# Optimization experiments

Measured on AMD Instinct MI355X. Metric: run time of the kernel, lower is better.

The kernel has to match this reference:

```python
import jax, jax.numpy as jnp
import numpy as np

# Static segment boundaries: lengths [512,512,512] + remainder -> ranges below
SEG_RANGES = [(0, 512), (512, 1024), (1024, 1536), (1536, 2048)]

B, N, D, H = 8, 2048, 1024, 2048
NUM_SEG = len(SEG_RANGES)


def setup_inputs() -> dict:
    key = jax.random.key(0)
    k_x, k1, k2, k3 = jax.random.split(key, 4)
    scale_in = 1.0 / np.sqrt(D)
    scale_h = 1.0 / np.sqrt(H)
    return {
        "x": jax.random.normal(k_x, (B, N, D), dtype=jnp.float32),
        "w1": jax.random.normal(k1, (NUM_SEG, D, H), dtype=jnp.float32) * scale_in,
        "w3": jax.random.normal(k2, (NUM_SEG, D, H), dtype=jnp.float32) * scale_in,
        "w2": jax.random.normal(k3, (NUM_SEG, H, D), dtype=jnp.float32) * scale_h,
    }


def reference(x, w1, w3, w2):
    # Per-segment independent SwiGLU FFN: out_seg = (silu(x W1) * (x W3)) W2
    outs = []
    for i, (s, e) in enumerate(SEG_RANGES):
        seg = jax.lax.dynamic_slice_in_dim(x, s, e - s, axis=-2)  # [B, L_i, D]
        h = jax.nn.silu(jnp.einsum('bld,dh->blh', seg, w1[i])) \
            * jnp.einsum('bld,dh->blh', seg, w3[i])               # [B, L_i, H]
        outs.append(jnp.einsum('blh,hd->bld', h, w2[i]))          # [B, L_i, D]
    # Segments tile [0, N) exactly, so concat == the .at[s:e].set() scatter loop
    return jnp.concatenate(outs, axis=-2)
```

## Files before the change

kernel.cpp:

```cpp
#include <hip/hip_runtime.h>
#include <hip/hip_bf16.h>

typedef __bf16 bf16_t;
typedef __attribute__((ext_vector_type(8))) __bf16 bf16x8;
typedef __attribute__((ext_vector_type(4))) float f32x4;

#define MFMA16(a, b, c) __builtin_amdgcn_mfma_f32_16x16x32_bf16((a), (b), (c), 0, 0, 0)

__device__ __forceinline__ unsigned short f2bf(float f) {
    bf16_t b = (bf16_t)f;
    return __builtin_bit_cast(unsigned short, b);
}

__device__ __forceinline__ void gload16(const void* g, void* l) {
    __builtin_amdgcn_global_load_lds(
        (const __attribute__((address_space(1))) void*)g,
        (__attribute__((address_space(3))) void*)l,
        16, 0, 0);
}

__device__ __forceinline__ void stage_tile(const bf16_t* __restrict__ g, int ld,
                                           bf16_t* lds, int tid) {
#pragma unroll
    for (int p = 0; p < 4; ++p) {
        int row = p * 32 + (tid >> 3);
        int c = (tid & 7) ^ (row & 7);
        gload16(g + (size_t)row * ld + c * 8, lds + p * 2048 + tid * 8);
    }
}

__device__ __forceinline__ bf16x8 read_frag(const bf16_t* lds, int r, int chunk) {
    int s = chunk ^ (r & 7);
    return *(const bf16x8*)(lds + r * 64 + s * 8);
}

__global__ __launch_bounds__(256) void cvtx(const float* __restrict__ src,
                                            bf16_t* __restrict__ dst) {
    size_t i = ((size_t)blockIdx.x * 256 + threadIdx.x) * 8;
    f32x4 v0 = *(const f32x4*)(src + i);
    f32x4 v1 = *(const f32x4*)(src + i + 4);
    bf16x8 o;
    o[0] = (bf16_t)v0[0]; o[1] = (bf16_t)v0[1];
    o[2] = (bf16_t)v0[2]; o[3] = (bf16_t)v0[3];
    o[4] = (bf16_t)v1[0]; o[5] = (bf16_t)v1[1];
    o[6] = (bf16_t)v1[2]; o[7] = (bf16_t)v1[3];
    *(bf16x8*)(dst + i) = o;
}

__global__ __launch_bounds__(256) void transcvt64(const float* __restrict__ src,
                                                  unsigned short* __restrict__ dst,
                                                  int R, int C) {
    __shared__ __align__(16) unsigned short tile[64][66];
    size_t off = (size_t)blockIdx.z * R * C;
    const float* s = src + off;
    unsigned short* d = dst + off;
    int tr = blockIdx.y * 64, tc = blockIdx.x * 64;
    int tid = threadIdx.x;
    int lr = tid >> 4;
    int lc = (tid & 15) * 4;
#pragma unroll
    for (int p = 0; p < 4; ++p) {
        int r = p * 16 + lr;
        f32x4 v = *(const f32x4*)(s + (size_t)(tr + r) * C + tc + lc);
        tile[r][lc + 0] = f2bf(v[0]); tile[r][lc + 1] = f2bf(v[1]);
        tile[r][lc + 2] = f2bf(v[2]); tile[r][lc + 3] = f2bf(v[3]);
    }
    __syncthreads();
#pragma unroll
    for (int p = 0; p < 4; ++p) {
        int oc = p * 16 + lr;
        ushort4 v;
        v.x = tile[lc + 0][oc]; v.y = tile[lc + 1][oc];
        v.z = tile[lc + 2][oc]; v.w = tile[lc + 3][oc];
        *(ushort4*)(d + (size_t)(tc + oc) * R + tr + lc) = v;
    }
}

__global__ __launch_bounds__(256, 3) void gemm13(const bf16_t* __restrict__ Xb,
                                                 const bf16_t* __restrict__ W1t,
                                                 const bf16_t* __restrict__ W3t,
                                                 bf16_t* __restrict__ Hh,
                                                 int row_base) {
    const int K = 1024, N = 2048;
    int row0 = blockIdx.x * 128;
    int col0 = blockIdx.y * 128;
    int seg = ((row_base + row0) & 2047) >> 9;
    const bf16_t* A  = Xb + (size_t)row0 * K;
    const bf16_t* B1 = W1t + (size_t)seg * N * K + (size_t)col0 * K;
    const bf16_t* B3 = W3t + (size_t)seg * N * K + (size_t)col0 * K;

    __shared__ __align__(16) bf16_t smem[3 * 128 * 64];
    bf16_t* sA  = smem;
    bf16_t* sB1 = smem + 8192;
    bf16_t* sB3 = smem + 16384;

    int tid = threadIdx.x;
    int lane = tid & 63, wave = tid >> 6;
    int wm = wave & 1, wn = wave >> 1;
    int quad = lane >> 4, l16 = lane & 15;

    f32x4 accU[4][4], accV[4][4];
    f32x4 z = {0.f, 0.f, 0.f, 0.f};
#pragma unroll
    for (int i = 0; i < 4; ++i)
#pragma unroll
        for (int j = 0; j < 4; ++j) { accU[i][j] = z; accV[i][j] = z; }

    for (int kt = 0; kt < K / 64; ++kt) {
        __syncthreads();
        stage_tile(A + kt * 64, K, sA, tid);
        stage_tile(B1 + kt * 64, K, sB1, tid);
        stage_tile(B3 + kt * 64, K, sB3, tid);
        __syncthreads();
#pragma unroll
        for (int kk = 0; kk < 2; ++kk) {
            int chunk = kk * 4 + quad;
            bf16x8 af[4], b1f[4], b3f[4];
#pragma unroll
            for (int i = 0; i < 4; ++i) af[i] = read_frag(sA, wm * 64 + i * 16 + l16, chunk);
#pragma unroll
            for (int j = 0; j < 4; ++j) b1f[j] = read_frag(sB1, wn * 64 + j * 16 + l16, chunk);
#pragma unroll
            for (int j = 0; j < 4; ++j) b3f[j] = read_frag(sB3, wn * 64 + j * 16 + l16, chunk);
#pragma unroll
            for (int i = 0; i < 4; ++i)
#pragma unroll
                for (int j = 0; j < 4; ++j) {
                    accU[i][j] = MFMA16(af[i], b1f[j], accU[i][j]);
                    accV[i][j] = MFMA16(af[i], b3f[j], accV[i][j]);
                }
        }
    }

    __syncthreads();
    bf16_t* Ct = smem;
#pragma unroll
    for (int i = 0; i < 4; ++i)
#pragma unroll
        for (int j = 0; j < 4; ++j) {
            int r = wm * 64 + i * 16 + quad * 4;
            int c = wn * 64 + j * 16 + l16;
#pragma unroll
            for (int t = 0; t < 4; ++t) {
                float u = accU[i][j][t];
                float v = accV[i][j][t];
                float h = (u / (1.f + __expf(-u))) * v;
                Ct[(r + t) * 136 + c] = (bf16_t)h;
            }
        }
    __syncthreads();
#pragma unroll
    for (int s = 0; s < 8; ++s) {
        int r = s * 16 + wave * 4 + (lane >> 4);
        int cb = (lane & 15) * 8;
        bf16x8 v = *(const bf16x8*)(Ct + r * 136 + cb);
        *(bf16x8*)(Hh + (size_t)(row0 + r) * N + col0 + cb) = v;
    }
}

__global__ __launch_bounds__(256, 3) void gemm2k(const bf16_t* __restrict__ Hh,
                                                 const bf16_t* __restrict__ W2t,
                                                 float* __restrict__ Outc,
                                                 int row_base) {
    const int K = 2048, N = 1024;
    int row0 = blockIdx.x * 128;
    int col0 = blockIdx.y * 128;
    int seg = ((row_base + row0) & 2047) >> 9;
    const bf16_t* A = Hh + (size_t)row0 * K;
    const bf16_t* B = W2t + (size_t)seg * N * K + (size_t)col0 * K;

    __shared__ __align__(16) float smemf[64 * 130];
    bf16_t* sA = (bf16_t*)smemf;
    bf16_t* sB = sA + 8192;

    int tid = threadIdx.x;
    int lane = tid & 63, wave = tid >> 6;
    int wm = wave & 1, wn = wave >> 1;
    int quad = lane >> 4, l16 = lane & 15;

    f32x4 acc[4][4];
    f32x4 z = {0.f, 0.f, 0.f, 0.f};
#pragma unroll
    for (int i = 0; i < 4; ++i)
#pragma unroll
        for (int j = 0; j < 4; ++j) acc[i][j] = z;

    for (int kt = 0; kt < K / 64; ++kt) {
        __syncthreads();
        stage_tile(A + kt * 64, K, sA, tid);
        stage_tile(B + kt * 64, K, sB, tid);
        __syncthreads();
#pragma unroll
        for (int kk = 0; kk < 2; ++kk) {
            int chunk = kk * 4 + quad;
            bf16x8 af[4], bf[4];
#pragma unroll
            for (int i = 0; i < 4; ++i) af[i] = read_frag(sA, wm * 64 + i * 16 + l16, chunk);
#pragma unroll
            for (int j = 0; j < 4; ++j) bf[j] = read_frag(sB, wn * 64 + j * 16 + l16, chunk);
#pragma unroll
            for (int i = 0; i < 4; ++i)
#pragma unroll
                for (int j = 0; j < 4; ++j)
                    acc[i][j] = MFMA16(af[i], bf[j], acc[i][j]);
        }
    }

    for (int pass = 0; pass < 2; ++pass) {
        __syncthreads();
        if (wm == pass) {
#pragma unroll
            for (int i = 0; i < 4; ++i)
#pragma unroll
                for (int j = 0; j < 4; ++j) {
                    int r = i * 16 + quad * 4;
                    int c = wn * 64 + j * 16 + l16;
#pragma unroll
                    for (int t = 0; t < 4; ++t)
                        smemf[(r + t) * 130 + c] = acc[i][j][t];
                }
        }
        __syncthreads();
#pragma unroll
        for (int s = 0; s < 8; ++s) {
            int r = s * 8 + wave * 2 + (lane >> 5);
            int cb = (lane & 31) * 4;
            f32x4 v = *(const f32x4*)(smemf + r * 130 + cb);
            *(f32x4*)(Outc + (size_t)(row0 + pass * 64 + r) * N + col0 + cb) = v;
        }
    }
}

extern "C" void kernel_launch(void* const* d_in, const int* in_sizes, int n_in,
                              void* d_out, int out_size, void* d_ws, size_t ws_size,
                              hipStream_t stream) {
    const float* x  = (const float*)d_in[0];
    const float* w1 = (const float*)d_in[1];
    const float* w3 = (const float*)d_in[2];
    const float* w2 = (const float*)d_in[3];
    float* out = (float*)d_out;

    const size_t WSEG = (size_t)4 * 1024 * 2048;
    bf16_t* w1t = (bf16_t*)d_ws;
    bf16_t* w3t = w1t + WSEG;
    bf16_t* w2t = w3t + WSEG;
    bf16_t* dyn = w2t + WSEG;

    transcvt64<<<dim3(32, 16, 4), 256, 0, stream>>>(w1, (unsigned short*)w1t, 1024, 2048);
    transcvt64<<<dim3(32, 16, 4), 256, 0, stream>>>(w3, (unsigned short*)w3t, 1024, 2048);
    transcvt64<<<dim3(16, 32, 4), 256, 0, stream>>>(w2, (unsigned short*)w2t, 2048, 1024);

    const int TOTAL_ROWS = 16384;
    size_t wbytes = 3 * WSEG * sizeof(bf16_t);
    size_t avail = (ws_size > wbytes) ? ws_size - wbytes : 0;
    int chunk_rows = TOTAL_ROWS;
    while (chunk_rows > 128 && (size_t)chunk_rows * 6144 > avail)
        chunk_rows >>= 1;

    for (int rb = 0; rb < TOTAL_ROWS; rb += chunk_rows) {
        bf16_t* Xb = dyn;
        bf16_t* Hh = dyn + (size_t)chunk_rows * 1024;
        cvtx<<<chunk_rows / 2, 256, 0, stream>>>(x + (size_t)rb * 1024, Xb);
        gemm13<<<dim3(chunk_rows / 128, 16), 256, 0, stream>>>(
            Xb, w1t, w3t, Hh, rb);
        gemm2k<<<dim3(chunk_rows / 128, 8), 256, 0, stream>>>(
            Hh, w2t, out + (size_t)rb * 1024, rb);
    }
}
```

Before: 424.4 us.

## Rewrite both GEMMs with 512-thread tiles and double-buffered phased LDS pipeline

```diff
diff --git a/kernel.cpp b/kernel.cpp
--- a/kernel.cpp
+++ b/kernel.cpp
@@ -17,21 +17,6 @@
         (const __attribute__((address_space(1))) void*)g,
         (__attribute__((address_space(3))) void*)l,
         16, 0, 0);
-}
-
-__device__ __forceinline__ void stage_tile(const bf16_t* __restrict__ g, int ld,
-                                           bf16_t* lds, int tid) {
-#pragma unroll
-    for (int p = 0; p < 4; ++p) {
-        int row = p * 32 + (tid >> 3);
-        int c = (tid & 7) ^ (row & 7);
-        gload16(g + (size_t)row * ld + c * 8, lds + p * 2048 + tid * 8);
-    }
-}
-
-__device__ __forceinline__ bf16x8 read_frag(const bf16_t* lds, int r, int chunk) {
-    int s = chunk ^ (r & 7);
-    return *(const bf16x8*)(lds + r * 64 + s * 8);
 }
 
 __global__ __launch_bounds__(256) void cvtx(const float* __restrict__ src,
@@ -76,28 +61,42 @@
     }
 }
 
-__global__ __launch_bounds__(256, 3) void gemm13(const bf16_t* __restrict__ Xb,
+
+#define PH_FENCE { __builtin_amdgcn_sched_barrier(0); asm volatile("" ::: "memory"); }
+
+__global__ __launch_bounds__(512, 2) void gemm13(const bf16_t* __restrict__ Xb,
                                                  const bf16_t* __restrict__ W1t,
                                                  const bf16_t* __restrict__ W3t,
                                                  bf16_t* __restrict__ Hh,
                                                  int row_base) {
-    const int K = 1024, N = 2048;
-    int row0 = blockIdx.x * 128;
-    int col0 = blockIdx.y * 128;
+    const int K = 1024, N = 2048, KT = 16;
+    int nwg = gridDim.x, id = blockIdx.x;
+    if ((nwg & 7) == 0) id = (id & 7) * (nwg >> 3) + (id >> 3);
+    int nbx = nwg >> 4;
+    int bx = id % nbx, by = id / nbx;
+    int row0 = bx * 256, col0 = by * 128;
     int seg = ((row_base + row0) & 2047) >> 9;
-    const bf16_t* A  = Xb + (size_t)row0 * K;
-    const bf16_t* B1 = W1t + (size_t)seg * N * K + (size_t)col0 * K;
-    const bf16_t* B3 = W3t + (size_t)seg * N * K + (size_t)col0 * K;
-
-    __shared__ __align__(16) bf16_t smem[3 * 128 * 64];
+    const bf16_t* Ag  = Xb + (size_t)row0 * K;
+    const bf16_t* B1g = W1t + ((size_t)seg * N + col0) * K;
+    const bf16_t* B3g = W3t + ((size_t)seg * N + col0) * K;
+
+    __shared__ __align__(16) bf16_t smem[65536];
     bf16_t* sA  = smem;
-    bf16_t* sB1 = smem + 8192;
-    bf16_t* sB3 = smem + 16384;
-
-    int tid = threadIdx.x;
-    int lane = tid & 63, wave = tid >> 6;
-    int wm = wave & 1, wn = wave >> 1;
+    bf16_t* sB1 = smem + 32768;
+    bf16_t* sB3 = smem + 49152;
+
+    int tid = threadIdx.x, lane = tid & 63, w = tid >> 6;
+    int wm = w >> 1, wn = w & 1;
     int quad = lane >> 4, l16 = lane & 15;
+
+    int r0 = 2 * (tid >> 3) + ((tid >> 2) & 1);
+    int c0 = (tid & 3) ^ ((tid >> 3) & 3);
+    int offG  = r0 * K + c0 * 8;
+    int offG2 = offG + 128 * K;
+
+    int sigRd = ((l16 & 1) << 2) | (quad ^ ((l16 >> 1) & 3));
+    int rdA = (wm * 32 + (l16 >> 1)) * 64 + sigRd * 8;
+    int rdB = (wn * 32 + (l16 >> 1)) * 64 + sigRd * 8;
 
     f32x4 accU[4][4], accV[4][4];
     f32x4 z = {0.f, 0.f, 0.f, 0.f};
@@ -106,31 +105,71 @@
 #pragma unroll
         for (int j = 0; j < 4; ++j) { accU[i][j] = z; accV[i][j] = z; }
 
-    for (int kt = 0; kt < K / 64; ++kt) {
-        __syncthreads();
-        stage_tile(A + kt * 64, K, sA, tid);
-        stage_tile(B1 + kt * 64, K, sB1, tid);
-        stage_tile(B3 + kt * 64, K, sB3, tid);
-        __syncthreads();
-#pragma unroll
-        for (int kk = 0; kk < 2; ++kk) {
-            int chunk = kk * 4 + quad;
-            bf16x8 af[4], b1f[4], b3f[4];
-#pragma unroll
-            for (int i = 0; i < 4; ++i) af[i] = read_frag(sA, wm * 64 + i * 16 + l16, chunk);
-#pragma unroll
-            for (int j = 0; j < 4; ++j) b1f[j] = read_frag(sB1, wn * 64 + j * 16 + l16, chunk);
-#pragma unroll
-            for (int j = 0; j < 4; ++j) b3f[j] = read_frag(sB3, wn * 64 + j * 16 + l16, chunk);
-#pragma unroll
-            for (int i = 0; i < 4; ++i)
-#pragma unroll
-                for (int j = 0; j < 4; ++j) {
-                    accU[i][j] = MFMA16(af[i], b1f[j], accU[i][j]);
-                    accV[i][j] = MFMA16(af[i], b3f[j], accV[i][j]);
-                }
-        }
-    }
+    bf16x8 af0[4], af1[4], bfr[4];
+
+#define STGA13(k0, dst) { gload16(Ag + (k0) + offG, (dst) + tid * 8); \
+                          gload16(Ag + (k0) + offG2, (dst) + 4096 + tid * 8); }
+#define STGB13(gb, k0, dst) { gload16((gb) + (k0) + offG, (dst) + tid * 8); }
+
+#define PH13(d, ks, SBASE, AF, RDA, ACC, STAGE, WAITA) {                        \
+    PH_FENCE;                                                                   \
+    if (RDA) {                                                                  \
+        _Pragma("unroll")                                                       \
+        for (int i_ = 0; i_ < 4; ++i_)                                          \
+            AF[i_] = *(const bf16x8*)(sA + (d) * 16384 + (ks) * 8192 + rdA + i_ * 512); \
+    }                                                                           \
+    _Pragma("unroll")                                                           \
+    for (int j_ = 0; j_ < 4; ++j_)                                              \
+        bfr[j_] = *(const bf16x8*)((SBASE) + (d) * 8192 + (ks) * 4096 + rdB + j_ * 512); \
+    STAGE;                                                                      \
+    WAITA;                                                                      \
+    __builtin_amdgcn_s_barrier();                                               \
+    asm volatile("s_waitcnt lgkmcnt(0)" ::: "memory");                          \
+    __builtin_amdgcn_sched_barrier(0);                                          \
+    __builtin_amdgcn_s_setprio(1);                                              \
+    _Pragma("unroll")                                                           \
+    for (int i_ = 0; i_ < 4; ++i_)                                              \
+        _Pragma("unroll")                                                       \
+        for (int j_ = 0; j_ < 4; ++j_)                                          \
+            ACC[i_][j_] = MFMA16(AF[i_], bfr[j_], ACC[i_][j_]);                 \
+    __builtin_amdgcn_s_setprio(0);                                              \
+    __builtin_amdgcn_s_barrier();                                               \
+}
+
+#define TILE13(d, kn) {                                                         \
+    PH13(d, 0, sB1, af0, 1, accU,                                               \
+         { STGA13(kn, sA + (1 - (d)) * 16384);                                  \
+           STGB13(B1g, kn, sB1 + (1 - (d)) * 8192); },                          \
+         asm volatile("s_waitcnt vmcnt(5)" ::: "memory"));                      \
+    PH13(d, 1, sB1, af1, 1, accU,                                               \
+         { STGA13((kn) + 32, sA + (1 - (d)) * 16384 + 8192);                    \
+           STGB13(B1g, (kn) + 32, sB1 + (1 - (d)) * 8192 + 4096); },            \
+         asm volatile("s_waitcnt vmcnt(7)" ::: "memory"));                      \
+    PH13(d, 0, sB3, af0, 0, accV,                                               \
+         { STGB13(B3g, kn, sB3 + (1 - (d)) * 8192); },                          \
+         asm volatile("s_waitcnt vmcnt(7)" ::: "memory"));                      \
+    PH13(d, 1, sB3, af1, 0, accV,                                               \
+         { STGB13(B3g, (kn) + 32, sB3 + (1 - (d)) * 8192 + 4096); },            \
+         asm volatile("s_waitcnt vmcnt(5)" ::: "memory"));                      \
+}
+
+    STGA13(0, sA); STGB13(B1g, 0, sB1);
+    STGA13(32, sA + 8192); STGB13(B1g, 32, sB1 + 4096);
+    STGB13(B3g, 0, sB3); STGB13(B3g, 32, sB3 + 4096);
+    asm volatile("s_waitcnt vmcnt(5)" ::: "memory");
+    __builtin_amdgcn_s_barrier();
+
+    int kt = 0;
+#pragma unroll 1
+    for (; kt + 2 < KT; kt += 2) {
+        TILE13(0, (kt + 1) * 64);
+        TILE13(1, (kt + 2) * 64);
+    }
+    TILE13(0, (kt + 1) * 64);
+    PH13(1, 0, sB1, af0, 1, accU, , asm volatile("s_waitcnt vmcnt(2)" ::: "memory"));
+    PH13(1, 1, sB1, af1, 1, accU, , asm volatile("s_waitcnt vmcnt(1)" ::: "memory"));
+    PH13(1, 0, sB3, af0, 0, accV, , asm volatile("s_waitcnt vmcnt(0)" ::: "memory"));
+    PH13(1, 1, sB3, af1, 0, accV, , );
 
     __syncthreads();
     bf16_t* Ct = smem;
@@ -151,64 +190,120 @@
     __syncthreads();
 #pragma unroll
     for (int s = 0; s < 8; ++s) {
-        int r = s * 16 + wave * 4 + (lane >> 4);
-        int cb = (lane & 15) * 8;
+        int r = s * 32 + (tid >> 4);
+        int cb = (tid & 15) * 8;
         bf16x8 v = *(const bf16x8*)(Ct + r * 136 + cb);
         *(bf16x8*)(Hh + (size_t)(row0 + r) * N + col0 + cb) = v;
     }
-}
-
-__global__ __launch_bounds__(256, 3) void gemm2k(const bf16_t* __restrict__ Hh,
+#undef TILE13
+#undef PH13
+#undef STGA13
+#undef STGB13
+}
+
+__global__ __launch_bounds__(512, 2) void gemm2k(const bf16_t* __restrict__ Hh,
                                                  const bf16_t* __restrict__ W2t,
                                                  float* __restrict__ Outc,
                                                  int row_base) {
-    const int K = 2048, N = 1024;
-    int row0 = blockIdx.x * 128;
-    int col0 = blockIdx.y * 128;
+    const int K = 2048, N = 1024, KT = 32;
+    int nwg = gridDim.x, id = blockIdx.x;
+    if ((nwg & 7) == 0) id = (id & 7) * (nwg >> 3) + (id >> 3);
+    int nbx = nwg >> 2;
+    int bx = id % nbx, by = id / nbx;
+    int row0 = bx * 256, col0 = by * 256;
     int seg = ((row_base + row0) & 2047) >> 9;
-    const bf16_t* A = Hh + (size_t)row0 * K;
-    const bf16_t* B = W2t + (size_t)seg * N * K + (size_t)col0 * K;
-
-    __shared__ __align__(16) float smemf[64 * 130];
-    bf16_t* sA = (bf16_t*)smemf;
-    bf16_t* sB = sA + 8192;
-
-    int tid = threadIdx.x;
-    int lane = tid & 63, wave = tid >> 6;
-    int wm = wave & 1, wn = wave >> 1;
+    const bf16_t* Ag = Hh + (size_t)row0 * K;
+    const bf16_t* Bg = W2t + ((size_t)seg * N + col0) * K;
+
+    __shared__ __align__(16) bf16_t smem[65536];
+    bf16_t* sA = smem;
+    bf16_t* sB = smem + 32768;
+
+    int tid = threadIdx.x, lane = tid & 63, w = tid >> 6;
+    int wm = w >> 2, wn = w & 3;
     int quad = lane >> 4, l16 = lane & 15;
 
-    f32x4 acc[4][4];
+    int r0 = 2 * (tid >> 3) + ((tid >> 2) & 1);
+    int c0 = (tid & 3) ^ ((tid >> 3) & 3);
+    int offG  = r0 * K + c0 * 8;
+    int offG2 = offG + 128 * K;
+
+    int sigRd = ((l16 & 1) << 2) | (quad ^ ((l16 >> 1) & 3));
+    int rdA = (wm * 64 + (l16 >> 1)) * 64 + sigRd * 8;
+    int rdB = (wn * 32 + (l16 >> 1)) * 64 + sigRd * 8;
+
+    f32x4 acc[8][4];
     f32x4 z = {0.f, 0.f, 0.f, 0.f};
 #pragma unroll
-    for (int i = 0; i < 4; ++i)
+    for (int i = 0; i < 8; ++i)
 #pragma unroll
         for (int j = 0; j < 4; ++j) acc[i][j] = z;
 
-    for (int kt = 0; kt < K / 64; ++kt) {
-        __syncthreads();
-        stage_tile(A + kt * 64, K, sA, tid);
-        stage_tile(B + kt * 64, K, sB, tid);
-        __syncthreads();
-#pragma unroll
-        for (int kk = 0; kk < 2; ++kk) {
-            int chunk = kk * 4 + quad;
-            bf16x8 af[4], bf[4];
-#pragma unroll
-            for (int i = 0; i < 4; ++i) af[i] = read_frag(sA, wm * 64 + i * 16 + l16, chunk);
-#pragma unroll
-            for (int j = 0; j < 4; ++j) bf[j] = read_frag(sB, wn * 64 + j * 16 + l16, chunk);
-#pragma unroll
-            for (int i = 0; i < 4; ++i)
-#pragma unroll
-                for (int j = 0; j < 4; ++j)
-                    acc[i][j] = MFMA16(af[i], bf[j], acc[i][j]);
-        }
-    }
-
-    for (int pass = 0; pass < 2; ++pass) {
-        __syncthreads();
-        if (wm == pass) {
+    bf16x8 bfr[4];
+
+#define STG2KA(k0, dst) { gload16(Ag + (k0) + offG, (dst) + tid * 8); \
+                          gload16(Ag + (k0) + offG2, (dst) + 4096 + tid * 8); }
+#define STG2KB(k0, dst) { gload16(Bg + (k0) + offG, (dst) + tid * 8); \
+                          gload16(Bg + (k0) + offG2, (dst) + 4096 + tid * 8); }
+
+#define PH2K(d, mq, ks, RDB, STAGE, WAITA) {                                    \
+    PH_FENCE;                                                                   \
+    bf16x8 af_[4];                                                              \
+    _Pragma("unroll")                                                           \
+    for (int i_ = 0; i_ < 4; ++i_)                                              \
+        af_[i_] = *(const bf16x8*)(sA + (d) * 16384 + (ks) * 8192 + rdA + (mq) * 2048 + i_ * 512); \
+    if (RDB) {                                                                  \
+        _Pragma("unroll")                                                       \
+        for (int j_ = 0; j_ < 4; ++j_)                                          \
+            bfr[j_] = *(const bf16x8*)(sB + (d) * 16384 + (ks) * 8192 + rdB + j_ * 512); \
+    }                                                                           \
+    STAGE;                                                                      \
+    WAITA;                                                                      \
+    __builtin_amdgcn_s_barrier();                                               \
+    asm volatile("s_waitcnt lgkmcnt(0)" ::: "memory");                          \
+    __builtin_amdgcn_sched_barrier(0);                                          \
+    __builtin_amdgcn_s_setprio(1);                                              \
+    _Pragma("unroll")                                                           \
+    for (int i_ = 0; i_ < 4; ++i_)                                              \
+        _Pragma("unroll")                                                       \
+        for (int j_ = 0; j_ < 4; ++j_)                                          \
+            acc[(mq) * 4 + i_][j_] = MFMA16(af_[i_], bfr[j_], acc[(mq) * 4 + i_][j_]); \
+    __builtin_amdgcn_s_setprio(0);                                              \
+    __builtin_amdgcn_s_barrier();                                               \
+}
+
+#define TILE2K(d, kn) {                                                         \
+    PH2K(d, 0, 0, 1, STG2KA(kn, sA + (1 - (d)) * 16384), );                     \
+    PH2K(d, 1, 0, 0, STG2KB(kn, sB + (1 - (d)) * 16384),                        \
+         asm volatile("s_waitcnt vmcnt(4)" ::: "memory"));                      \
+    PH2K(d, 0, 1, 1, STG2KA((kn) + 32, sA + (1 - (d)) * 16384 + 8192), );       \
+    PH2K(d, 1, 1, 0, STG2KB((kn) + 32, sB + (1 - (d)) * 16384 + 8192),          \
+         asm volatile("s_waitcnt vmcnt(4)" ::: "memory"));                      \
+}
+
+    STG2KA(0, sA); STG2KB(0, sB);
+    STG2KA(32, sA + 8192); STG2KB(32, sB + 8192);
+    asm volatile("s_waitcnt vmcnt(4)" ::: "memory");
+    __builtin_amdgcn_s_barrier();
+
+    int kt = 0;
+#pragma unroll 1
+    for (; kt + 2 < KT; kt += 2) {
+        TILE2K(0, (kt + 1) * 64);
+        TILE2K(1, (kt + 2) * 64);
+    }
+    TILE2K(0, (kt + 1) * 64);
+    PH2K(1, 0, 0, 1, , );
+    PH2K(1, 1, 0, 0, , asm volatile("s_waitcnt vmcnt(0)" ::: "memory"));
+    PH2K(1, 0, 1, 1, , );
+    PH2K(1, 1, 1, 0, , );
+
+    __syncthreads();
+    float* smemf = (float*)smem;
+    for (int pass = 0; pass < 4; ++pass) {
+        if (pass) __syncthreads();
+        if (wm == (pass >> 1)) {
+            int mq = pass & 1;
 #pragma unroll
             for (int i = 0; i < 4; ++i)
 #pragma unroll
@@ -217,18 +312,21 @@
                     int c = wn * 64 + j * 16 + l16;
 #pragma unroll
                     for (int t = 0; t < 4; ++t)
-                        smemf[(r + t) * 130 + c] = acc[i][j][t];
+                        smemf[(r + t) * 260 + c] = acc[mq * 4 + i][j][t];
                 }
         }
         __syncthreads();
 #pragma unroll
         for (int s = 0; s < 8; ++s) {
-            int r = s * 8 + wave * 2 + (lane >> 5);
-            int cb = (lane & 31) * 4;
-            f32x4 v = *(const f32x4*)(smemf + r * 130 + cb);
-            *(f32x4*)(Outc + (size_t)(row0 + pass * 64 + r) * N + col0 + cb) = v;
+            int r = s * 8 + w;
+            f32x4 v = *(const f32x4*)(smemf + r * 260 + lane * 4);
+            *(f32x4*)(Outc + (size_t)(row0 + pass * 64 + r) * N + col0 + lane * 4) = v;
         }
     }
+#undef TILE2K
+#undef PH2K
+#undef STG2KA
+#undef STG2KB
 }
 
 extern "C" void kernel_launch(void* const* d_in, const int* in_sizes, int n_in,
@@ -254,16 +352,14 @@
     size_t wbytes = 3 * WSEG * sizeof(bf16_t);
     size_t avail = (ws_size > wbytes) ? ws_size - wbytes : 0;
     int chunk_rows = TOTAL_ROWS;
-    while (chunk_rows > 128 && (size_t)chunk_rows * 6144 > avail)
+    while (chunk_rows > 256 && (size_t)chunk_rows * 6144 > avail)
         chunk_rows >>= 1;
 
     for (int rb = 0; rb < TOTAL_ROWS; rb += chunk_rows) {
         bf16_t* Xb = dyn;
         bf16_t* Hh = dyn + (size_t)chunk_rows * 1024;
         cvtx<<<chunk_rows / 2, 256, 0, stream>>>(x + (size_t)rb * 1024, Xb);
-        gemm13<<<dim3(chunk_rows / 128, 16), 256, 0, stream>>>(
-            Xb, w1t, w3t, Hh, rb);
-        gemm2k<<<dim3(chunk_rows / 128, 8), 256, 0, stream>>>(
-            Hh, w2t, out + (size_t)rb * 1024, rb);
-    }
-}
+        gemm13<<<(chunk_rows / 256) * 16, 512, 0, stream>>>(Xb, w1t, w3t, Hh, rb);
+        gemm2k<<<(chunk_rows / 256) * 4, 512, 0, stream>>>(Hh, w2t, out + (size_t)rb * 1024, rb);
+    }
+}
```

Measured after the change: 405.6 us. 1.05x faster.
